# Kernel tuning notes

Measured on AMD Instinct MI355X. Metric: run time of the kernel, lower is better.

Reference implementation:

```python
import jax, jax.numpy as jnp
import numpy as np

N = 100000      # nodes
E = 1600000     # edges (before self-loops)
F_IN = 128      # dataset.num_features
H1 = 128        # hidden_channels/2
H2 = 256        # hidden_channels
C = 40          # dataset.num_classes
EPS = 1e-5      # BatchNorm eps
NEG_SLOPE = 0.2 # GATConv leaky_relu slope


def setup_inputs() -> dict:
    key = jax.random.key(0)
    ks = jax.random.split(key, 12)
    p = lambda k, shape: jax.random.normal(k, shape, jnp.float32) * 0.1
    x = jax.random.normal(ks[0], (N, F_IN), jnp.float32)
    edge_index = jax.random.randint(ks[1], (2, E), 0, N, dtype=jnp.int64)
    return dict(
        x=x, edge_index=edge_index,
        w1=p(ks[2], (F_IN, H1)), as1=p(ks[3], (H1,)), ad1=p(ks[4], (H1,)), b1=jnp.zeros(H1, jnp.float32),
        g1=jnp.ones(H1, jnp.float32), be1=jnp.zeros(H1, jnp.float32), rm1=jnp.zeros(H1, jnp.float32), rv1=jnp.ones(H1, jnp.float32),
        w2=p(ks[5], (H1, H2)), as2=p(ks[6], (H2,)), ad2=p(ks[7], (H2,)), b2=jnp.zeros(H2, jnp.float32),
        g2=jnp.ones(H2, jnp.float32), be2=jnp.zeros(H2, jnp.float32), rm2=jnp.zeros(H2, jnp.float32), rv2=jnp.ones(H2, jnp.float32),
        w3=p(ks[8], (H2, C)), as3=p(ks[9], (C,)), ad3=p(ks[10], (C,)), b3=jnp.zeros(C, jnp.float32),
    )


def gat_conv(x, src, dst, W, a_src, a_dst, b):
    """PyG GATConv (heads=1, add_self_loops already applied to src/dst)."""
    h = x @ W                                  # [N, F_out]
    alpha_src = h @ a_src                      # [N]
    alpha_dst = h @ a_dst                      # [N]
    logits = jax.nn.leaky_relu(alpha_src[src] + alpha_dst[dst], NEG_SLOPE)  # [E']
    # segment softmax over incoming edges of each dst node
    m = jax.ops.segment_max(logits, dst, num_segments=N)
    e = jnp.exp(logits - m[dst])
    denom = jax.ops.segment_sum(e, dst, num_segments=N)
    alpha = e / denom[dst]                     # [E']
    out = jax.ops.segment_sum(h[src] * alpha[:, None], dst, num_segments=N)
    return out + b


def bn_eval(x, gamma, beta, mean, var):
    return (x - mean) * jax.lax.rsqrt(var + EPS) * gamma + beta


def reference(x, edge_index,
              w1, as1, ad1, b1, g1, be1, rm1, rv1,
              w2, as2, ad2, b2, g2, be2, rm2, rv2,
              w3, as3, ad3, b3):
    # add self-loops once (PyG GATConv default add_self_loops=True)
    loop = jnp.arange(N, dtype=edge_index.dtype)
    src = jnp.concatenate([edge_index[0], loop])
    dst = jnp.concatenate([edge_index[1], loop])
    # eval mode: dropout is identity, BN uses running stats
    h = gat_conv(x, src, dst, w1, as1, ad1, b1)
    h = jnp.tanh(bn_eval(h, g1, be1, rm1, rv1))
    h = gat_conv(h, src, dst, w2, as2, ad2, b2)
    h = jnp.tanh(bn_eval(h, g2, be2, rm2, rv2))
    return gat_conv(h, src, dst, w3, as3, ad3, b3)
```

## Files before the change

kernel.cpp:

```cpp
#include <hip/hip_runtime.h>
#include <hip/hip_bf16.h>
#include <cstddef>

#define N_NODES 100000
#define E_EDGES 1600000
#define TOT_EDGES (E_EDGES + N_NODES)
#define NEG_SLOPE 0.2f
#define BN_EPS 1e-5f
#define NBKT ((N_NODES + 255) / 256)
#define NBA 512

typedef __attribute__((ext_vector_type(8))) short short8;
typedef __attribute__((ext_vector_type(4))) float f32x4;
typedef __attribute__((ext_vector_type(2))) float f32x2;
typedef __attribute__((ext_vector_type(4))) int int32x4;
typedef __attribute__((ext_vector_type(2))) int int32x2;

#if defined(__has_builtin)
#if __has_builtin(__builtin_amdgcn_make_buffer_rsrc) && __has_builtin(__builtin_amdgcn_raw_buffer_load_b128)
#define HAVE_BUFRSRC 1
#endif
#if __has_builtin(__builtin_amdgcn_make_buffer_rsrc) && __has_builtin(__builtin_amdgcn_raw_buffer_load_b64)
#define HAVE_BUF64 1
#endif
#endif

__device__ __forceinline__ unsigned short f2bf(float f) {
    union { float f; unsigned u; } c; c.f = f;
    unsigned u = c.u;
    u += 0x7fffu + ((u >> 16) & 1u);
    return (unsigned short)(u >> 16);
}
__device__ __forceinline__ float bf2f(unsigned short h) {
    union { unsigned u; float f; } c; c.u = ((unsigned)h) << 16;
    return c.f;
}
__device__ __forceinline__ unsigned short f2h(float f) {
    union { _Float16 h; unsigned short u; } c; c.h = (_Float16)f; return c.u;
}
__device__ __forceinline__ float lrelu(float t) {
    return (t > 0.f) ? t : NEG_SLOPE * t;
}
__device__ __forceinline__ float tanh_fast(float x) {
    float e = __expf(2.f * x);
    return 1.f - 2.f / (e + 1.f);
}
__device__ __forceinline__ unsigned short pk_fp8(float a, float b) {
    unsigned v;
    asm volatile("v_cvt_pk_fp8_f32 %0, %1, %2" : "=v"(v) : "v"(a), "v"(b));
    return (unsigned short)v;
}
__device__ __forceinline__ f32x2 unpk_fp8(unsigned u) {
    f32x2 r;
    asm volatile("v_cvt_pk_f32_fp8 %0, %1" : "=v"(r) : "v"(u));
    return r;
}

__device__ __forceinline__ int xcd_chunk_swz(int b, int nwg) {
    int q = nwg >> 3, r = nwg & 7, xb = b & 7, ib = b >> 3;
    return (xb < r ? xb * (q + 1) : r * (q + 1) + (xb - r) * q) + ib;
}

__device__ __forceinline__ float wave_sum63(float x) {
    x += __int_as_float(__builtin_amdgcn_update_dpp(0, __float_as_int(x), 0x111, 0xf, 0xf, true));
    x += __int_as_float(__builtin_amdgcn_update_dpp(0, __float_as_int(x), 0x112, 0xf, 0xf, true));
    x += __int_as_float(__builtin_amdgcn_update_dpp(0, __float_as_int(x), 0x114, 0xf, 0xf, true));
    x += __int_as_float(__builtin_amdgcn_update_dpp(0, __float_as_int(x), 0x118, 0xf, 0xf, true));
    x += __int_as_float(__builtin_amdgcn_update_dpp(0, __float_as_int(x), 0x142, 0xf, 0xf, true));
    x += __int_as_float(__builtin_amdgcn_update_dpp(0, __float_as_int(x), 0x143, 0xf, 0xf, true));
    return x;
}
__device__ __forceinline__ float wave_sum_bcast(float x) {
    return __int_as_float(__builtin_amdgcn_readlane(__float_as_int(wave_sum63(x)), 63));
}


__global__ __launch_bounds__(256) void csr_hist(const int* __restrict__ ei,
                                                int* __restrict__ bh) {
    __shared__ int h[NBKT];
    int t = threadIdx.x;
    for (int b = t; b < NBKT; b += 256) h[b] = 0;
    __syncthreads();
    int idx = blockIdx.x * 256 + t;
    const int stride = NBA * 256;
    for (int e = idx; e < TOT_EDGES; e += stride) {
        int d = (e < E_EDGES) ? ei[E_EDGES + e] : (e - E_EDGES);
        atomicAdd(&h[((unsigned)d) >> 8], 1);
    }
    __syncthreads();
    for (int b = t; b < NBKT; b += 256) bh[blockIdx.x * NBKT + b] = h[b];
}

__global__ __launch_bounds__(512) void csr_scan_blocks(int* __restrict__ bh,
                                                       int* __restrict__ totals) {
    __shared__ int s[NBA];
    int t = threadIdx.x, bin = blockIdx.x;
    int v = bh[t * NBKT + bin];
    s[t] = v;
    __syncthreads();
    for (int off = 1; off < NBA; off <<= 1) {
        int y = (t >= off) ? s[t - off] : 0;
        __syncthreads();
        s[t] += y;
        __syncthreads();
    }
    bh[t * NBKT + bin] = s[t] - v;
    if (t == NBA - 1) totals[bin] = s[t];
}

__global__ __launch_bounds__(512) void csr_scan_buckets(const int* __restrict__ totals,
                                                        int* __restrict__ starts) {
    __shared__ int s[512];
    int t = threadIdx.x;
    int v = (t < NBKT) ? totals[t] : 0;
    s[t] = v;
    __syncthreads();
    for (int off = 1; off < 512; off <<= 1) {
        int y = (t >= off) ? s[t - off] : 0;
        __syncthreads();
        s[t] += y;
        __syncthreads();
    }
    if (t < NBKT) starts[t] = s[t] - v;
    if (t == 0) starts[NBKT] = TOT_EDGES;
}

__global__ __launch_bounds__(256) void csr_scatter(const int* __restrict__ ei,
                                                   const int* __restrict__ bh,
                                                   const int* __restrict__ starts,
                                                   int* __restrict__ pairs) {
    __shared__ int wp[NBKT];
    int t = threadIdx.x;
    for (int b = t; b < NBKT; b += 256)
        wp[b] = starts[b] + bh[blockIdx.x * NBKT + b];
    __syncthreads();
    int idx = blockIdx.x * 256 + t;
    const int stride = NBA * 256;
    for (int e = idx; e < TOT_EDGES; e += stride) {
        int s, d;
        if (e < E_EDGES) { s = ei[e]; d = ei[E_EDGES + e]; }
        else             { s = e - E_EDGES; d = s; }
        int pos = atomicAdd(&wp[((unsigned)d) >> 8], 1);
        pairs[pos] = s | ((d & 255) << 20);
    }
}

__global__ __launch_bounds__(256) void csr_build(const int* __restrict__ pairs,
                                                 const int* __restrict__ starts,
                                                 int* __restrict__ row_ptr,
                                                 int* __restrict__ src_sorted) {
    __shared__ int nh[256];
    __shared__ int sc[256];
    __shared__ int wp[256];
    int k = blockIdx.x, t = threadIdx.x;
    int bs = starts[k], be = starts[k + 1];
    nh[t] = 0;
    __syncthreads();
    for (int i = bs + t; i < be; i += 256)
        atomicAdd(&nh[((unsigned)pairs[i]) >> 20], 1);
    __syncthreads();
    int v = nh[t];
    sc[t] = v;
    __syncthreads();
    for (int off = 1; off < 256; off <<= 1) {
        int y = (t >= off) ? sc[t - off] : 0;
        __syncthreads();
        sc[t] += y;
        __syncthreads();
    }
    int excl = sc[t] - v;
    int node = k * 256 + t;
    if (node <= N_NODES) row_ptr[node] = bs + excl;
    wp[t] = bs + excl;
    __syncthreads();
    for (int i = bs + t; i < be; i += 256) {
        unsigned p = (unsigned)pairs[i];
        int pos = atomicAdd(&wp[p >> 20], 1);
        src_sorted[pos] = (int)(p & 0xFFFFFu);
    }
}

__global__ __launch_bounds__(256) void wprep_all(
    const float* __restrict__ w1, const float* __restrict__ w2, const float* __restrict__ w3,
    const float* __restrict__ as1, const float* __restrict__ ad1,
    const float* __restrict__ as2, const float* __restrict__ ad2,
    const float* __restrict__ as3, const float* __restrict__ ad3,
    const float* __restrict__ b2a, const float* __restrict__ g2a,
    const float* __restrict__ be2a, const float* __restrict__ rm2a,
    const float* __restrict__ rv2a,
    unsigned short* __restrict__ w1th, unsigned short* __restrict__ w1tl,
    unsigned short* __restrict__ w2th, unsigned short* __restrict__ w2tl,
    unsigned short* __restrict__ w3th, unsigned short* __restrict__ w3tl,
    unsigned short* __restrict__ ab1h, unsigned short* __restrict__ ab1l,
    unsigned short* __restrict__ ab3h, unsigned short* __restrict__ ab3l,
    float* __restrict__ ws2f, float* __restrict__ wd2f,
    float* __restrict__ bn2S, float* __restrict__ bn2T) {
    const int T1 = 128 * 128, T2 = 256 * 128, T3 = 48 * 256;
    const int W = T1 + T2 + T3;
    int idx = blockIdx.x * 256 + threadIdx.x;
    if (idx < W) {
        float v; unsigned short* th; unsigned short* tl; int o;
        if (idx < T1) {
            int n = idx / 128, k = idx % 128;
            v = w1[k * 128 + n]; th = w1th; tl = w1tl; o = idx;
        } else if (idx < T1 + T2) {
            int i = idx - T1; int n = i / 128, k = i % 128;
            v = w2[k * 256 + n]; th = w2th; tl = w2tl; o = i;
        } else {
            int i = idx - T1 - T2; int n = i / 256, k = i % 256;
            v = (n < 40) ? w3[k * 40 + n] : 0.f; th = w3th; tl = w3tl; o = i;
        }
        unsigned short h = f2bf(v);
        th[o] = h;
        tl[o] = f2bf(v - bf2f(h));
        return;
    }
    int j = idx - W;
    if (j < 2048) {
        int r = j / 128, k = j % 128;
        float v = 0.f;
        if (r < 2) {
            const float* a = r ? ad1 : as1;
            const float* wr = w1 + (size_t)k * 128;
            for (int n = 0; n < 128; n++) v += wr[n] * a[n];
        }
        unsigned short h = f2bf(v);
        ab1h[j] = h; ab1l[j] = f2bf(v - bf2f(h));
    } else if (j < 2048 + 4096) {
        int i = j - 2048; int r = i / 256, k = i % 256;
        float v = 0.f;
        if (r < 2) {
            const float* a = r ? ad3 : as3;
            const float* wr = w3 + (size_t)k * 40;
            for (int n = 0; n < 40; n++) v += wr[n] * a[n];
        }
        unsigned short h = f2bf(v);
        ab3h[i] = h; ab3l[i] = f2bf(v - bf2f(h));
    } else if (j < 2048 + 4096 + 256) {
        int i = j - 2048 - 4096; int r = i / 128, k = i % 128;
        const float* a = r ? ad2 : as2;
        const float* wr = w2 + (size_t)k * 256;
        float v = 0.f;
        for (int n = 0; n < 256; n++) v += wr[n] * a[n];
        if (r == 0) ws2f[k] = v; else wd2f[k] = v;
    } else if (j < 2048 + 4096 + 256 + 256) {
        int i = j - 2048 - 4096 - 256;
        float S = rsqrtf(rv2a[i] + BN_EPS) * g2a[i];
        bn2S[i] = S;
        bn2T[i] = (b2a[i] - rm2a[i]) * S + be2a[i];
    }
}

template<int K, int NTILES, int MWAVES, int NWAVES, int NACT, bool ASPLIT, bool ALPHA, bool BNT, bool CFRAG, bool CHALF, bool AF32>
__global__ __launch_bounds__(256) void mfma_gemm(
    const unsigned short* __restrict__ Ahi, const unsigned short* __restrict__ Alo,
    const unsigned short* __restrict__ BThi, const unsigned short* __restrict__ BTlo,
    const unsigned short* __restrict__ ABh, const unsigned short* __restrict__ ABl,
    unsigned short* __restrict__ Chi, int ldc,
    const float* __restrict__ bias, const float* __restrict__ gamma,
    const float* __restrict__ beta, const float* __restrict__ rmean,
    const float* __restrict__ rvar,
    float* __restrict__ asrc, float* __restrict__ adst, int M)
{
    int lane = threadIdx.x & 63;
    int wave = threadIdx.x >> 6;
    int quad = lane >> 4;
    int l16  = lane & 15;
    long mbase = (long)blockIdx.x * (64 * MWAVES) + (long)(wave / NWAVES) * 64;
    int n0 = ((wave % NWAVES) + blockIdx.y * NWAVES) * (NTILES * 16);
    bool aw = ((wave % NWAVES) == 0) && (blockIdx.y == 0);
    const size_t CSTRIDE = (size_t)M * 32;

    size_t roff[4];
#pragma unroll
    for (int i = 0; i < 4; i++) {
        long r = mbase + i * 16 + l16;
        if (r > M - 1) r = M - 1;
        roff[i] = AF32 ? ((size_t)r * K + (size_t)(quad * 8))
                       : ((size_t)r * 32 + (size_t)(quad * 8));
    }
    const unsigned short* bh[NTILES]; const unsigned short* bl[NTILES];
#pragma unroll
    for (int j = 0; j < NTILES; j++) {
        long n = n0 + j * 16 + l16;
        bh[j] = BThi + n * K; bl[j] = BTlo + n * K;
    }
    const unsigned short* bah = nullptr; const unsigned short* bal = nullptr;
    if constexpr (ALPHA) { bah = ABh + (size_t)l16 * K; bal = ABl + (size_t)l16 * K; }
    const int ko = quad * 8;

    f32x4 acc[4][NTILES];
    f32x4 acca[4];
#pragma unroll
    for (int i = 0; i < 4; i++) {
        acca[i] = (f32x4){0.f, 0.f, 0.f, 0.f};
#pragma unroll
        for (int j = 0; j < NTILES; j++)
            acc[i][j] = (f32x4){0.f, 0.f, 0.f, 0.f};
    }

    for (int kc = 0; kc < K / 32; kc++) {
        const int k0 = kc * 32;
        short8 vah[4], vall[4], vbh[NTILES], vbl[NTILES];
#pragma unroll
        for (int i = 0; i < 4; i++) {
            if constexpr (AF32) {
                const float* xf = (const float*)Ahi;
                const float* pa = xf + roff[i] + kc * 32;
                f32x4 va = *(const f32x4*)pa;
                f32x4 vb = *(const f32x4*)(pa + 4);
#pragma unroll
                for (int q = 0; q < 8; q++) {
                    float v = (q < 4) ? va[q] : vb[q - 4];
                    unsigned short h = f2bf(v);
                    vah[i][q] = (short)h;
                    vall[i][q] = (short)f2bf(v - bf2f(h));
                }
            } else {
                const unsigned short* Ah = Ahi + (size_t)kc * CSTRIDE;
                vah[i] = *(const short8*)(Ah + roff[i]);
                if constexpr (ASPLIT) {
                    const unsigned short* Al = Alo + (size_t)kc * CSTRIDE;
                    vall[i] = *(const short8*)(Al + roff[i]);
                }
            }
        }
#pragma unroll
        for (int j = 0; j < NTILES; j++) {
            vbh[j] = *(const short8*)(bh[j] + k0 + ko);
            vbl[j] = *(const short8*)(bl[j] + k0 + ko);
        }
#pragma unroll
        for (int i = 0; i < 4; i++)
#pragma unroll
            for (int j = 0; j < NTILES; j++) {
                acc[i][j] = __builtin_amdgcn_mfma_f32_16x16x32_bf16(vah[i], vbh[j], acc[i][j], 0, 0, 0);
                acc[i][j] = __builtin_amdgcn_mfma_f32_16x16x32_bf16(vah[i], vbl[j], acc[i][j], 0, 0, 0);
                if constexpr (ASPLIT)
                    acc[i][j] = __builtin_amdgcn_mfma_f32_16x16x32_bf16(vall[i], vbh[j], acc[i][j], 0, 0, 0);
            }
        if constexpr (ALPHA) {
            if (aw) {
                short8 vbah = *(const short8*)(bah + k0 + ko);
                short8 vbal = *(const short8*)(bal + k0 + ko);
#pragma unroll
                for (int i = 0; i < 4; i++) {
                    acca[i] = __builtin_amdgcn_mfma_f32_16x16x32_bf16(vah[i], vbah, acca[i], 0, 0, 0);
                    acca[i] = __builtin_amdgcn_mfma_f32_16x16x32_bf16(vah[i], vbal, acca[i], 0, 0, 0);
                    if constexpr (ASPLIT)
                        acca[i] = __builtin_amdgcn_mfma_f32_16x16x32_bf16(vall[i], vbah, acca[i], 0, 0, 0);
                }
            }
        }
    }

#pragma unroll
    for (int i = 0; i < 4; i++)
#pragma unroll
        for (int j = 0; j < NTILES; j++) {
            int col = n0 + j * 16 + l16;
            float bb = 0.f, rs = 1.f, gg = 1.f, bt = 0.f, rm = 0.f;
            if constexpr (BNT) {
                bb = bias[col]; gg = gamma[col]; bt = beta[col];
                rm = rmean[col]; rs = rsqrtf(rvar[col] + BN_EPS);
            }
#pragma unroll
            for (int r = 0; r < 4; r++) {
                long row = mbase + i * 16 + quad * 4 + r;
                if (row < M && col < NACT) {
                    float v = acc[i][j][r];
                    if constexpr (BNT) v = tanh_fast((v + bb - rm) * rs * gg + bt);
                    if constexpr (CFRAG) {
                        Chi[(size_t)(col >> 5) * CSTRIDE + (size_t)row * 32 + (col & 31)] = f2bf(v);
                    } else {
                        Chi[row * ldc + col] = CHALF ? f2h(v) : f2bf(v);
                    }
                }
            }
        }
    if constexpr (ALPHA) {
        if (aw) {
#pragma unroll
            for (int i = 0; i < 4; i++)
#pragma unroll
                for (int r = 0; r < 4; r++) {
                    long row = mbase + i * 16 + quad * 4 + r;
                    if (row < M) {
                        float v = acca[i][r];
                        if (l16 == 0) asrc[row] = v;
                        else if (l16 == 1) adst[row] = v;
                    }
                }
        }
    }
}

__global__ __launch_bounds__(512) void gemm23_fused(
    const unsigned short* __restrict__ Ahi,
    const unsigned short* __restrict__ B2h, const unsigned short* __restrict__ B2l,
    const float* __restrict__ bnS, const float* __restrict__ bnT,
    const unsigned short* __restrict__ B3h, const unsigned short* __restrict__ B3l,
    const unsigned short* __restrict__ AB3h, const unsigned short* __restrict__ AB3l,
    unsigned short* __restrict__ h3,
    float* __restrict__ asrc, float* __restrict__ adst, int M)
{
    constexpr int LW = 40;
    __shared__ unsigned short o2l[8 * 64 * LW];

    int lane = threadIdx.x & 63;
    int wave = threadIdx.x >> 6;
    int quad = lane >> 4;
    int l16  = lane & 15;
    int g = xcd_chunk_swz(blockIdx.x, gridDim.x);
    long mbase = (long)g * 64;
    const size_t CSTRIDE = (size_t)M * 32;
    const int ko = quad * 8;

    size_t roff[4];
#pragma unroll
    for (int i = 0; i < 4; i++) {
        long r = mbase + i * 16 + l16;
        if (r > M - 1) r = M - 1;
        roff[i] = (size_t)r * 32 + (size_t)ko;
    }
    int n0 = wave * 32;
    const unsigned short* bh[2]; const unsigned short* bl[2];
#pragma unroll
    for (int j = 0; j < 2; j++) {
        long n = n0 + j * 16 + l16;
        bh[j] = B2h + n * 128; bl[j] = B2l + n * 128;
    }

    f32x4 acc[4][2];
#pragma unroll
    for (int i = 0; i < 4; i++)
#pragma unroll
        for (int j = 0; j < 2; j++)
            acc[i][j] = (f32x4){0.f, 0.f, 0.f, 0.f};

#pragma unroll
    for (int kc = 0; kc < 4; kc++) {
        const int k0 = kc * 32;
        const unsigned short* Ah = Ahi + (size_t)kc * CSTRIDE;
        short8 vah[4], vbh[2], vbl[2];
#pragma unroll
        for (int i = 0; i < 4; i++) vah[i] = *(const short8*)(Ah + roff[i]);
#pragma unroll
        for (int j = 0; j < 2; j++) {
            vbh[j] = *(const short8*)(bh[j] + k0 + ko);
            vbl[j] = *(const short8*)(bl[j] + k0 + ko);
        }
#pragma unroll
        for (int i = 0; i < 4; i++)
#pragma unroll
            for (int j = 0; j < 2; j++) {
                acc[i][j] = __builtin_amdgcn_mfma_f32_16x16x32_bf16(vah[i], vbh[j], acc[i][j], 0, 0, 0);
                acc[i][j] = __builtin_amdgcn_mfma_f32_16x16x32_bf16(vah[i], vbl[j], acc[i][j], 0, 0, 0);
            }
    }

#pragma unroll
    for (int j = 0; j < 2; j++) {
        int col = n0 + j * 16 + l16;
        float S = bnS[col], T = bnT[col];
        int cbase = (col >> 5) * 64 * LW + (col & 31);
#pragma unroll
        for (int i = 0; i < 4; i++)
#pragma unroll
            for (int r = 0; r < 4; r++) {
                int li = i * 16 + quad * 4 + r;
                o2l[cbase + li * LW] = f2bf(tanh_fast(acc[i][j][r] * S + T));
            }
    }
    __syncthreads();

    int rh   = wave >> 2;
    int task = wave & 3;
    int lrow0 = rh * 32 + l16;
    int lrow1 = rh * 32 + 16 + l16;

    const unsigned short* p3h;
    const unsigned short* p3l;
    if (task < 3) {
        p3h = B3h + (size_t)(task * 16 + l16) * 256;
        p3l = B3l + (size_t)(task * 16 + l16) * 256;
    } else {
        p3h = AB3h + (size_t)l16 * 256;
        p3l = AB3l + (size_t)l16 * 256;
    }

    f32x4 a3[2][2];
#pragma unroll
    for (int i = 0; i < 2; i++)
#pragma unroll
        for (int pp = 0; pp < 2; pp++)
            a3[i][pp] = (f32x4){0.f, 0.f, 0.f, 0.f};

#pragma unroll
    for (int kc = 0; kc < 8; kc++) {
        const int k0 = kc * 32;
        const int par = kc & 1;
        short8 a0 = *(const short8*)(o2l + (kc * 64 + lrow0) * LW + ko);
        short8 a1 = *(const short8*)(o2l + (kc * 64 + lrow1) * LW + ko);
        short8 vh = *(const short8*)(p3h + k0 + ko);
        short8 vl = *(const short8*)(p3l + k0 + ko);
        a3[0][par] = __builtin_amdgcn_mfma_f32_16x16x32_bf16(a0, vh, a3[0][par], 0, 0, 0);
        a3[0][par] = __builtin_amdgcn_mfma_f32_16x16x32_bf16(a0, vl, a3[0][par], 0, 0, 0);
        a3[1][par] = __builtin_amdgcn_mfma_f32_16x16x32_bf16(a1, vh, a3[1][par], 0, 0, 0);
        a3[1][par] = __builtin_amdgcn_mfma_f32_16x16x32_bf16(a1, vl, a3[1][par], 0, 0, 0);
    }
    f32x4 r3[2];
    r3[0] = a3[0][0] + a3[0][1];
    r3[1] = a3[1][0] + a3[1][1];

    if (task < 3) {
        int col = task * 16 + l16;
#pragma unroll
        for (int i = 0; i < 2; i++)
#pragma unroll
            for (int r = 0; r < 4; r++) {
                long row = mbase + rh * 32 + i * 16 + quad * 4 + r;
                if (row < M) h3[(size_t)row * 64 + col] = f2h(r3[i][r]);
            }
    } else {
#pragma unroll
        for (int i = 0; i < 2; i++)
#pragma unroll
            for (int r = 0; r < 4; r++) {
                long row = mbase + rh * 32 + i * 16 + quad * 4 + r;
                if (row < M) {
                    if (l16 == 0) asrc[row] = r3[i][r];
                    else if (l16 == 1) adst[row] = r3[i][r];
                }
            }
    }
}

template<int MODE, int SWZ>
__global__ __launch_bounds__(256) void gat_agg_wide(
    const unsigned short* __restrict__ hsrc,
    const float* __restrict__ asrc, const float* __restrict__ adst,
    const int* __restrict__ row_ptr, const int* __restrict__ src_sorted,
    const float* __restrict__ bias, const float* __restrict__ gamma,
    const float* __restrict__ beta, const float* __restrict__ rmean,
    const float* __restrict__ rvar,
    const float* __restrict__ wsn, const float* __restrict__ wdn,
    unsigned short* __restrict__ ohi,
    float* __restrict__ outf,
    float* __restrict__ asrc_n, float* __restrict__ adst_n)
{
    constexpr int SH  = (MODE == 0) ? 8 : 7;
    constexpr int BPL = (MODE == 0) ? 16 : 8;
    constexpr int NF  = (MODE == 2) ? 4 : 8;

    __shared__ __align__(16) float2 esw[4][64];
    __shared__ __align__(16) float red[4][4][132];

    int wave = threadIdx.x >> 6;
    int lane = threadIdx.x & 63;
    int bId = blockIdx.x;
    if constexpr (SWZ) bId = xcd_chunk_swz(bId, gridDim.x);
    int node = bId * 4 + wave;
    if (node >= N_NODES) return;

    int start = row_ptr[node];
    int end = row_ptr[node + 1];
    int deg = end - start;
    float ad = adst[node];
    int sub = lane >> 4;
    int foff = (lane & 15) * BPL;
    int tpos = (lane & 3) * 16 + (lane >> 2);

#if defined(HAVE_BUFRSRC) && defined(HAVE_BUF64)
    auto rsrc = __builtin_amdgcn_make_buffer_rsrc((void*)hsrc, (short)0,
                                                  N_NODES << SH, 0x00020000);
#endif

    float acc[NF];
#pragma unroll
    for (int i = 0; i < NF; i++) acc[i] = 0.f;

    auto ld = [&](int vo) {
        if constexpr (MODE == 0) {
#if defined(HAVE_BUFRSRC) && defined(HAVE_BUF64)
            return __builtin_amdgcn_raw_buffer_load_b128(rsrc, vo, 0, 0);
#else
            return *reinterpret_cast<const int32x4*>(
                reinterpret_cast<const char*>(hsrc) + (unsigned)vo);
#endif
        } else {
#if defined(HAVE_BUFRSRC) && defined(HAVE_BUF64)
            return __builtin_amdgcn_raw_buffer_load_b64(rsrc, vo, 0, 0);
#else
            return *reinterpret_cast<const int32x2*>(
                reinterpret_cast<const char*>(hsrc) + (unsigned)vo);
#endif
        }
    };
    auto fmaN = [&](auto u, float ww) {
        if constexpr (MODE == 0) {
            union { decltype(u) v; unsigned w[4]; } c; c.v = u;
#pragma unroll
            for (int i = 0; i < 4; i++) {
                union { unsigned u; _Float16 h[2]; } t; t.u = c.w[i];
                acc[2 * i]     += ww * (float)t.h[0];
                acc[2 * i + 1] += ww * (float)t.h[1];
            }
        } else if constexpr (MODE == 1) {
            union { decltype(u) v; unsigned w[2]; } c; c.v = u;
#pragma unroll
            for (int i = 0; i < 2; i++) {
                f32x2 lo = unpk_fp8(c.w[i]);
                f32x2 hi = unpk_fp8(c.w[i] >> 16);
                acc[4 * i]     += ww * lo.x;
                acc[4 * i + 1] += ww * lo.y;
                acc[4 * i + 2] += ww * hi.x;
                acc[4 * i + 3] += ww * hi.y;
            }
        } else {
            union { decltype(u) v; unsigned w[2]; } c; c.v = u;
#pragma unroll
            for (int i = 0; i < 2; i++) {
                union { unsigned u; _Float16 h[2]; } t; t.u = c.w[i];
                acc[2 * i]     += ww * (float)t.h[0];
                acc[2 * i + 1] += ww * (float)t.h[1];
            }
        }
    };
    auto gather = [&](int nst) {
        const float2* ep = &esw[wave][sub * 16];
#pragma unroll
        for (int b = 0; b < 4; b++) {
            int s0 = b * 4;
            if (s0 < nst) {
                f32x4 p01 = *(const f32x4*)(ep + s0);
                f32x4 p23 = *(const f32x4*)(ep + s0 + 2);
                bool g1 = s0 + 1 < nst, g2 = s0 + 2 < nst, g3 = s0 + 3 < nst;
                auto u0 = ld(__float_as_int(p01.x) + foff);
                decltype(u0) u1, u2, u3;
                if (g1) u1 = ld(__float_as_int(p01.z) + foff);
                if (g2) u2 = ld(__float_as_int(p23.x) + foff);
                if (g3) u3 = ld(__float_as_int(p23.z) + foff);
                fmaN(u0, p01.y);
                if (g1) fmaN(u1, p01.w);
                if (g2) fmaN(u2, p23.y);
                if (g3) fmaN(u3, p23.w);
            }
        }
    };

    if (deg <= 64) {
        int e = start + lane;
        int s = 0; float w = 0.f;
        if (e < end) { s = src_sorted[e]; w = __expf(lrelu(asrc[s] + ad)); }
        float dsum = wave_sum_bcast(w);
        esw[wave][tpos] = make_float2(__int_as_float(s << SH), w * (1.0f / dsum));
        gather((deg + 3) >> 2);
    } else {
        float part = 0.f;
        for (int cs = start; cs < end; cs += 64) {
            int e = cs + lane;
            if (e < end) part += __expf(lrelu(asrc[src_sorted[e]] + ad));
        }
        float inv = 1.0f / wave_sum_bcast(part);
        for (int cs = start; cs < end; cs += 64) {
            int e = cs + lane;
            int s = 0; float w = 0.f;
            if (e < end) { s = src_sorted[e]; w = __expf(lrelu(asrc[s] + ad)) * inv; }
            esw[wave][tpos] = make_float2(__int_as_float(s << SH), w);
            gather((min(64, end - cs) + 3) >> 2);
        }
    }

    if constexpr (MODE == 2) {
        *reinterpret_cast<f32x4*>(&red[wave][sub][(lane & 15) * 4]) =
            (f32x4){acc[0], acc[1], acc[2], acc[3]};
        float t = 0.f;
#pragma unroll
        for (int g = 0; g < 4; g++) t += red[wave][g][lane];
        if (lane < 40) outf[(size_t)node * 40 + lane] = t + bias[lane];
    } else {
        f32x4* dst = reinterpret_cast<f32x4*>(&red[wave][sub][(lane & 15) * 8]);
        dst[0] = (f32x4){acc[0], acc[1], acc[2], acc[3]};
        dst[1] = (f32x4){acc[4], acc[5], acc[6], acc[7]};
        f32x2 tsum = (f32x2){0.f, 0.f};
#pragma unroll
        for (int g = 0; g < 4; g++)
            tsum += *reinterpret_cast<const f32x2*>(&red[wave][g][lane * 2]);

        if constexpr (MODE == 0) {
            float vals[2];
#pragma unroll
            for (int v = 0; v < 2; v++) {
                int f = lane * 2 + v;
                float val = tsum[v] + bias[f];
                float rs = rsqrtf(rvar[f] + BN_EPS);
                vals[v] = tanh_fast((val - rmean[f]) * rs * gamma[f] + beta[f]);
            }
            ohi[(size_t)node * 64 + lane] = pk_fp8(vals[0], vals[1]);
            float ps = vals[0] * wsn[lane * 2] + vals[1] * wsn[lane * 2 + 1];
            float pd = vals[0] * wdn[lane * 2] + vals[1] * wdn[lane * 2 + 1];
            ps = wave_sum63(ps);
            pd = wave_sum63(pd);
            if (lane == 63) { asrc_n[node] = ps; adst_n[node] = pd; }
        } else {
            const size_t CSTRIDE = (size_t)N_NODES * 32;
            unsigned w0 = (unsigned)f2bf(tsum[0]) | ((unsigned)f2bf(tsum[1]) << 16);
            size_t a = (size_t)(lane >> 4) * CSTRIDE + (size_t)node * 32 + ((lane * 2) & 31);
            *reinterpret_cast<unsigned*>(ohi + a) = w0;
        }
    }
}


static inline size_t align256(size_t x) { return (x + 255) & ~(size_t)255; }

extern "C" void kernel_launch(void* const* d_in, const int* in_sizes, int n_in,
                              void* d_out, int out_size, void* d_ws, size_t ws_size,
                              hipStream_t stream) {
    const float* x   = (const float*)d_in[0];
    const int* ei    = (const int*)d_in[1];
    const float* w1  = (const float*)d_in[2];
    const float* as1 = (const float*)d_in[3];
    const float* ad1 = (const float*)d_in[4];
    const float* b1  = (const float*)d_in[5];
    const float* g1  = (const float*)d_in[6];
    const float* be1 = (const float*)d_in[7];
    const float* rm1 = (const float*)d_in[8];
    const float* rv1 = (const float*)d_in[9];
    const float* w2  = (const float*)d_in[10];
    const float* as2 = (const float*)d_in[11];
    const float* ad2 = (const float*)d_in[12];
    const float* b2  = (const float*)d_in[13];
    const float* g2  = (const float*)d_in[14];
    const float* be2 = (const float*)d_in[15];
    const float* rm2 = (const float*)d_in[16];
    const float* rv2 = (const float*)d_in[17];
    const float* w3  = (const float*)d_in[18];
    const float* as3 = (const float*)d_in[19];
    const float* ad3 = (const float*)d_in[20];
    const float* b3  = (const float*)d_in[21];
    float* out = (float*)d_out;

    const size_t P128 = align256((size_t)N_NODES * 128 * 2);
    const size_t P256 = align256((size_t)N_NODES * 256 * 2);

    char* p = (char*)d_ws;
    char* regA = p; p += P256;
    char* regB = p; p += P256;
    unsigned short* o1p  = (unsigned short*)regA;
    unsigned short* h3h  = (unsigned short*)regA;
    unsigned short* h1h  = (unsigned short*)regB;
    unsigned short* g2hi = (unsigned short*)regB;
    int* pairs  = (int*)regB;
    int* bhist  = (int*)(regB + align256((size_t)TOT_EDGES * 4));
    int* totals = (int*)((char*)bhist + align256((size_t)NBA * NBKT * 4));
    int* starts = (int*)((char*)totals + align256((size_t)NBKT * 4));

    float* asrcA = (float*)p; p += align256((size_t)N_NODES * 4);
    float* adstA = (float*)p; p += align256((size_t)N_NODES * 4);
    float* asrcB = (float*)p; p += align256((size_t)N_NODES * 4);
    float* adstB = (float*)p; p += align256((size_t)N_NODES * 4);
    int* row_ptr   = (int*)p; p += align256((size_t)(N_NODES + 1) * 4);
    int* src_sorted = (int*)p; p += align256((size_t)TOT_EDGES * 4);
    unsigned short* w1th = (unsigned short*)p; p += align256(128 * 128 * 2);
    unsigned short* w1tl = (unsigned short*)p; p += align256(128 * 128 * 2);
    unsigned short* w2th = (unsigned short*)p; p += align256(256 * 128 * 2);
    unsigned short* w2tl = (unsigned short*)p; p += align256(256 * 128 * 2);
    unsigned short* w3th = (unsigned short*)p; p += align256(48 * 256 * 2);
    unsigned short* w3tl = (unsigned short*)p; p += align256(48 * 256 * 2);
    unsigned short* ab1h = (unsigned short*)p; p += align256(16 * 128 * 2);
    unsigned short* ab1l = (unsigned short*)p; p += align256(16 * 128 * 2);
    unsigned short* ab3h = (unsigned short*)p; p += align256(16 * 256 * 2);
    unsigned short* ab3l = (unsigned short*)p; p += align256(16 * 256 * 2);
    float* ws2f = (float*)p; p += align256(128 * 4);
    float* wd2f = (float*)p; p += align256(128 * 4);
    float* bn2S = (float*)p; p += align256(256 * 4);
    float* bn2T = (float*)p; p += align256(256 * 4);

    const int WTOT = 128 * 128 + 256 * 128 + 48 * 256 + 2048 + 4096 + 256 + 256;

    wprep_all<<<(WTOT + 255) / 256, 256, 0, stream>>>(
        w1, w2, w3, as1, ad1, as2, ad2, as3, ad3,
        b2, g2, be2, rm2, rv2,
        w1th, w1tl, w2th, w2tl, w3th, w3tl,
        ab1h, ab1l, ab3h, ab3l, ws2f, wd2f, bn2S, bn2T);

    csr_hist<<<NBA, 256, 0, stream>>>(ei, bhist);
    csr_scan_blocks<<<NBKT, 512, 0, stream>>>(bhist, totals);
    csr_scan_buckets<<<1, 512, 0, stream>>>(totals, starts);
    csr_scatter<<<NBA, 256, 0, stream>>>(ei, bhist, starts, pairs);
    csr_build<<<NBKT, 256, 0, stream>>>(pairs, starts, row_ptr, src_sorted);

    const int NWB = (N_NODES + 3) / 4;
    const int G64 = (N_NODES + 63) / 64;

    mfma_gemm<128, 2, 1, 4, 128, true, true, false, false, true, true><<<G64, 256, 0, stream>>>(
        (const unsigned short*)x, nullptr, w1th, w1tl, ab1h, ab1l, h1h, 128,
        nullptr, nullptr, nullptr, nullptr, nullptr, asrcA, adstA, N_NODES);
    gat_agg_wide<0, 0><<<NWB, 256, 0, stream>>>(
        h1h, asrcA, adstA, row_ptr, src_sorted,
        b1, g1, be1, rm1, rv1, ws2f, wd2f,
        o1p, nullptr, asrcB, adstB);

    gat_agg_wide<1, 1><<<NWB, 256, 0, stream>>>(
        o1p, asrcB, adstB, row_ptr, src_sorted,
        nullptr, nullptr, nullptr, nullptr, nullptr, nullptr, nullptr,
        g2hi, nullptr, nullptr, nullptr);

    gemm23_fused<<<G64, 512, 0, stream>>>(
        g2hi, w2th, w2tl, bn2S, bn2T,
        w3th, w3tl, ab3h, ab3l, h3h, asrcA, adstA, N_NODES);

    gat_agg_wide<2, 0><<<NWB, 256, 0, stream>>>(
        h3h, asrcA, adstA, row_ptr, src_sorted,
        b3, nullptr, nullptr, nullptr, nullptr, nullptr, nullptr,
        nullptr, out, nullptr, nullptr);
}
```

Before: 443.6 us.

## Shrink fused GEMM2/3 tile to 32 rows and drop XCD block swizzle

The fused layer-2/layer-3 GEMM kernel now processes 32 rows per block with 4 waves (each wave covering 64 output columns) instead of 64 rows with 8 waves, halving shared memory and doubling the grid. The XCD chunk swizzle is removed from both this kernel and the MODE-1 aggregation kernel, so blocks use plain linear indexing. The intent is to improve occupancy and load balance. In exchange, each block reloads the B weights for half as many rows, and the removed swizzle may reduce L2 locality across XCDs.

```diff
diff --git a/kernel.cpp b/kernel.cpp
--- a/kernel.cpp
+++ b/kernel.cpp
@@ -54,11 +54,6 @@
     f32x2 r;
     asm volatile("v_cvt_pk_f32_fp8 %0, %1" : "=v"(r) : "v"(u));
     return r;
-}
-
-__device__ __forceinline__ int xcd_chunk_swz(int b, int nwg) {
-    int q = nwg >> 3, r = nwg & 7, xb = b & 7, ib = b >> 3;
-    return (xb < r ? xb * (q + 1) : r * (q + 1) + (xb - r) * q) + ib;
 }
 
 __device__ __forceinline__ float wave_sum63(float x) {
@@ -395,7 +390,7 @@
     }
 }
 
-__global__ __launch_bounds__(512) void gemm23_fused(
+__global__ __launch_bounds__(256) void gemm23_fused(
     const unsigned short* __restrict__ Ahi,
     const unsigned short* __restrict__ B2h, const unsigned short* __restrict__ B2l,
     const float* __restrict__ bnS, const float* __restrict__ bnT,
@@ -405,67 +400,66 @@
     float* __restrict__ asrc, float* __restrict__ adst, int M)
 {
     constexpr int LW = 40;
-    __shared__ unsigned short o2l[8 * 64 * LW];
+    __shared__ unsigned short o2l[8 * 32 * LW];
 
     int lane = threadIdx.x & 63;
     int wave = threadIdx.x >> 6;
     int quad = lane >> 4;
     int l16  = lane & 15;
-    int g = xcd_chunk_swz(blockIdx.x, gridDim.x);
-    long mbase = (long)g * 64;
+    long mbase = (long)blockIdx.x * 32;
     const size_t CSTRIDE = (size_t)M * 32;
     const int ko = quad * 8;
 
-    size_t roff[4];
-#pragma unroll
-    for (int i = 0; i < 4; i++) {
+    size_t roff[2];
+#pragma unroll
+    for (int i = 0; i < 2; i++) {
         long r = mbase + i * 16 + l16;
         if (r > M - 1) r = M - 1;
         roff[i] = (size_t)r * 32 + (size_t)ko;
     }
-    int n0 = wave * 32;
-    const unsigned short* bh[2]; const unsigned short* bl[2];
-#pragma unroll
-    for (int j = 0; j < 2; j++) {
+    int n0 = wave * 64;
+    const unsigned short* bh[4]; const unsigned short* bl[4];
+#pragma unroll
+    for (int j = 0; j < 4; j++) {
         long n = n0 + j * 16 + l16;
         bh[j] = B2h + n * 128; bl[j] = B2l + n * 128;
     }
 
-    f32x4 acc[4][2];
-#pragma unroll
-    for (int i = 0; i < 4; i++)
-#pragma unroll
-        for (int j = 0; j < 2; j++)
+    f32x4 acc[2][4];
+#pragma unroll
+    for (int i = 0; i < 2; i++)
+#pragma unroll
+        for (int j = 0; j < 4; j++)
             acc[i][j] = (f32x4){0.f, 0.f, 0.f, 0.f};
 
 #pragma unroll
     for (int kc = 0; kc < 4; kc++) {
         const int k0 = kc * 32;
         const unsigned short* Ah = Ahi + (size_t)kc * CSTRIDE;
-        short8 vah[4], vbh[2], vbl[2];
-#pragma unroll
-        for (int i = 0; i < 4; i++) vah[i] = *(const short8*)(Ah + roff[i]);
-#pragma unroll
-        for (int j = 0; j < 2; j++) {
+        short8 vah[2], vbh[4], vbl[4];
+#pragma unroll
+        for (int i = 0; i < 2; i++) vah[i] = *(const short8*)(Ah + roff[i]);
+#pragma unroll
+        for (int j = 0; j < 4; j++) {
             vbh[j] = *(const short8*)(bh[j] + k0 + ko);
             vbl[j] = *(const short8*)(bl[j] + k0 + ko);
         }
 #pragma unroll
-        for (int i = 0; i < 4; i++)
-#pragma unroll
-            for (int j = 0; j < 2; j++) {
+        for (int i = 0; i < 2; i++)
+#pragma unroll
+            for (int j = 0; j < 4; j++) {
                 acc[i][j] = __builtin_amdgcn_mfma_f32_16x16x32_bf16(vah[i], vbh[j], acc[i][j], 0, 0, 0);
                 acc[i][j] = __builtin_amdgcn_mfma_f32_16x16x32_bf16(vah[i], vbl[j], acc[i][j], 0, 0, 0);
             }
     }
 
 #pragma unroll
-    for (int j = 0; j < 2; j++) {
+    for (int j = 0; j < 4; j++) {
         int col = n0 + j * 16 + l16;
         float S = bnS[col], T = bnT[col];
-        int cbase = (col >> 5) * 64 * LW + (col & 31);
-#pragma unroll
-        for (int i = 0; i < 4; i++)
+        int cbase = (col >> 5) * 32 * LW + (col & 31);
+#pragma unroll
+        for (int i = 0; i < 2; i++)
 #pragma unroll
             for (int r = 0; r < 4; r++) {
                 int li = i * 16 + quad * 4 + r;
@@ -474,10 +468,9 @@
     }
     __syncthreads();
 
-    int rh   = wave >> 2;
-    int task = wave & 3;
-    int lrow0 = rh * 32 + l16;
-    int lrow1 = rh * 32 + 16 + l16;
+    int task = wave;
+    int lrow0 = l16;
+    int lrow1 = 16 + l16;
 
     const unsigned short* p3h;
     const unsigned short* p3l;
@@ -500,8 +493,8 @@
     for (int kc = 0; kc < 8; kc++) {
         const int k0 = kc * 32;
         const int par = kc & 1;
-        short8 a0 = *(const short8*)(o2l + (kc * 64 + lrow0) * LW + ko);
-        short8 a1 = *(const short8*)(o2l + (kc * 64 + lrow1) * LW + ko);
+        short8 a0 = *(const short8*)(o2l + (kc * 32 + lrow0) * LW + ko);
+        short8 a1 = *(const short8*)(o2l + (kc * 32 + lrow1) * LW + ko);
         short8 vh = *(const short8*)(p3h + k0 + ko);
         short8 vl = *(const short8*)(p3l + k0 + ko);
         a3[0][par] = __builtin_amdgcn_mfma_f32_16x16x32_bf16(a0, vh, a3[0][par], 0, 0, 0);
@@ -519,7 +512,7 @@
         for (int i = 0; i < 2; i++)
 #pragma unroll
             for (int r = 0; r < 4; r++) {
-                long row = mbase + rh * 32 + i * 16 + quad * 4 + r;
+                long row = mbase + i * 16 + quad * 4 + r;
                 if (row < M) h3[(size_t)row * 64 + col] = f2h(r3[i][r]);
             }
     } else {
@@ -527,7 +520,7 @@
         for (int i = 0; i < 2; i++)
 #pragma unroll
             for (int r = 0; r < 4; r++) {
-                long row = mbase + rh * 32 + i * 16 + quad * 4 + r;
+                long row = mbase + i * 16 + quad * 4 + r;
                 if (row < M) {
                     if (l16 == 0) asrc[row] = r3[i][r];
                     else if (l16 == 1) adst[row] = r3[i][r];
@@ -536,7 +529,7 @@
     }
 }
 
-template<int MODE, int SWZ>
+template<int MODE>
 __global__ __launch_bounds__(256) void gat_agg_wide(
     const unsigned short* __restrict__ hsrc,
     const float* __restrict__ asrc, const float* __restrict__ adst,
@@ -558,9 +551,7 @@
 
     int wave = threadIdx.x >> 6;
     int lane = threadIdx.x & 63;
-    int bId = blockIdx.x;
-    if constexpr (SWZ) bId = xcd_chunk_swz(bId, gridDim.x);
-    int node = bId * 4 + wave;
+    int node = blockIdx.x * 4 + wave;
     if (node >= N_NODES) return;
 
     int start = row_ptr[node];
@@ -794,25 +785,26 @@
 
     const int NWB = (N_NODES + 3) / 4;
     const int G64 = (N_NODES + 63) / 64;
+    const int G32 = (N_NODES + 31) / 32;
 
     mfma_gemm<128, 2, 1, 4, 128, true, true, false, false, true, true><<<G64, 256, 0, stream>>>(
         (const unsigned short*)x, nullptr, w1th, w1tl, ab1h, ab1l, h1h, 128,
         nullptr, nullptr, nullptr, nullptr, nullptr, asrcA, adstA, N_NODES);
-    gat_agg_wide<0, 0><<<NWB, 256, 0, stream>>>(
+    gat_agg_wide<0><<<NWB, 256, 0, stream>>>(
         h1h, asrcA, adstA, row_ptr, src_sorted,
         b1, g1, be1, rm1, rv1, ws2f, wd2f,
         o1p, nullptr, asrcB, adstB);
 
-    gat_agg_wide<1, 1><<<NWB, 256, 0, stream>>>(
+    gat_agg_wide<1><<<NWB, 256, 0, stream>>>(
         o1p, asrcB, adstB, row_ptr, src_sorted,
         nullptr, nullptr, nullptr, nullptr, nullptr, nullptr, nullptr,
         g2hi, nullptr, nullptr, nullptr);
 
-    gemm23_fused<<<G64, 512, 0, stream>>>(
+    gemm23_fused<<<G32, 256, 0, stream>>>(
         g2hi, w2th, w2tl, bn2S, bn2T,
         w3th, w3tl, ab3h, ab3l, h3h, asrcA, adstA, N_NODES);
 
-    gat_agg_wide<2, 0><<<NWB, 256, 0, stream>>>(
+    gat_agg_wide<2><<<NWB, 256, 0, stream>>>(
         h3h, asrcA, adstA, row_ptr, src_sorted,
         b3, nullptr, nullptr, nullptr, nullptr, nullptr, nullptr,
         nullptr, out, nullptr, nullptr);
```

After: 444.3 us. About the same (+0.1%).
